# Performance work log

Hardware: AMD Instinct MI355X
Metric: run time of the kernel (lower is better)

Reference implementation:

```python
import jax, jax.numpy as jnp
import numpy as np

B, S, D_IN, D_OUT = 4, 2048, 4096, 4096
N_ADAPTERS, MAX_RANK = 8, 16


def setup_inputs() -> dict:
    key = jax.random.key(0)
    ks = jax.random.split(key, 7)
    x = jax.random.normal(ks[0], (B, S, D_IN), dtype=jnp.float32)
    weight = jax.random.normal(ks[1], (D_OUT, D_IN), dtype=jnp.float32) * (1.0 / np.sqrt(D_IN))
    bias = jax.random.normal(ks[2], (D_OUT,), dtype=jnp.float32) * 0.01
    lora_a_weights = jax.random.normal(ks[3], (N_ADAPTERS, MAX_RANK, D_IN), dtype=jnp.float32) * (1.0 / np.sqrt(D_IN))
    lora_b_weights = jax.random.normal(ks[4], (N_ADAPTERS, D_OUT, MAX_RANK), dtype=jnp.float32) * 0.02
    scaling_factors = jax.random.uniform(ks[5], (N_ADAPTERS,), dtype=jnp.float32, minval=0.5, maxval=2.0)
    adapter_id = jax.random.randint(ks[6], (B,), 0, N_ADAPTERS, dtype=jnp.int64)
    return {
        "x": x,
        "weight": weight,
        "bias": bias,
        "lora_a_weights": lora_a_weights,
        "lora_b_weights": lora_b_weights,
        "scaling_factors": scaling_factors,
        "adapter_id": adapter_id,
    }


def reference(x, weight, bias, lora_a_weights, lora_b_weights, scaling_factors, adapter_id):
    # Base linear: [B,S,Din] @ [Dout,Din]^T + bias -> [B,S,Dout]
    base = jnp.einsum('bsi,oi->bso', x, weight) + bias
    # Per-batch adapter gather (Punica/S-LoRA style bgmv)
    a_sel = lora_a_weights[adapter_id]      # [B, R, Din]
    b_sel = lora_b_weights[adapter_id]      # [B, Dout, R]
    scale = scaling_factors[adapter_id]     # [B]
    low = jnp.einsum('bsi,bri->bsr', x, a_sel)          # [B, S, R]
    delta = jnp.einsum('bsr,bor->bso', low, b_sel)      # [B, S, Dout]
    return base + scale[:, None, None] * delta
```

## Files before the change

### kernel.cpp

```cpp
#include <hip/hip_runtime.h>
#include <hip/hip_bf16.h>

#define BATCH 4
#define SEQ   2048
#define DIN   4096
#define DOUT  4096
#define MTOT  (BATCH * SEQ)
#define RANK  16

typedef __bf16 bf8_t  __attribute__((ext_vector_type(8)));
typedef float  f4_t   __attribute__((ext_vector_type(4)));

#define GLD_LDS(g, l) \
  __builtin_amdgcn_global_load_lds((const __attribute__((address_space(1))) void*)(g), \
                                   (__attribute__((address_space(3))) void*)(l), 16, 0, 0)

__global__ __launch_bounds__(256) void conv_w_kernel(
    const float* __restrict__ w, __bf16* __restrict__ wb) {
  const size_t i = ((size_t)blockIdx.x * 256 + threadIdx.x) * 8;
  f4_t a = *(const f4_t*)(w + i);
  f4_t b = *(const f4_t*)(w + i + 4);
  bf8_t o;
#pragma unroll
  for (int e = 0; e < 4; ++e) { o[e] = (__bf16)a[e]; o[4 + e] = (__bf16)b[e]; }
  *(bf8_t*)(wb + i) = o;
}

__global__ __launch_bounds__(256) void lora_low_kernel(
    const float* __restrict__ x, const float* __restrict__ Aw,
    const float* __restrict__ scales, const int* __restrict__ adapter_id,
    __bf16* __restrict__ xb, float* __restrict__ lowS) {
  const int t    = threadIdx.x;
  const int w    = t >> 6;
  const int lane = t & 63;
  const int quad = lane >> 4;
  const int l16  = lane & 15;
  const int m0   = blockIdx.x * 64;
  const int kb   = blockIdx.y * 512;
  const int b    = adapter_id[m0 >> 11];
  const float scale = scales[b];

  const int row = m0 + w * 16 + l16;
  const float*  xp  = x  + (size_t)row * DIN + kb + quad * 8;
  __bf16*       xbp = xb + (size_t)row * DIN + kb + quad * 8;
  const float*  ap  = Aw + ((size_t)b * RANK + l16) * DIN + kb + quad * 8;

  f4_t acc = (f4_t)0.f;
#pragma unroll 4
  for (int it = 0; it < 16; ++it) {
    const int off = it * 32;
    f4_t u0 = *(const f4_t*)(xp + off);
    f4_t u1 = *(const f4_t*)(xp + off + 4);
    f4_t v0 = *(const f4_t*)(ap + off);
    f4_t v1 = *(const f4_t*)(ap + off + 4);
    bf8_t af, bfr;
#pragma unroll
    for (int e = 0; e < 4; ++e) {
      af[e] = (__bf16)u0[e]; af[4 + e] = (__bf16)u1[e];
      bfr[e] = (__bf16)v0[e]; bfr[4 + e] = (__bf16)v1[e];
    }
    *(bf8_t*)(xbp + off) = af;
    acc = __builtin_amdgcn_mfma_f32_16x16x32_bf16(af, bfr, acc, 0, 0, 0);
  }
#pragma unroll
  for (int e = 0; e < 4; ++e)
    atomicAdd(&lowS[(size_t)(m0 + w * 16 + quad * 4 + e) * RANK + l16], acc[e] * scale);
}

#define BM 256
#define BN 256
#define BKT 64
#define NT (DIN / BKT)
#define NIT (NT / 2)

#define BAR() __builtin_amdgcn_s_barrier()
#define VMW(n) asm volatile("s_waitcnt vmcnt(" #n ")" ::: "memory")

__global__ __launch_bounds__(512, 2) void lora_gemm_kernel(
    const __bf16* __restrict__ x, const __bf16* __restrict__ wgt,
    const float* __restrict__ bias, const float* __restrict__ loraB,
    const int* __restrict__ adapter_id, const float* __restrict__ lowS,
    float* __restrict__ out) {
  __shared__ __bf16 lds[2][2][2][128 * 64];

  const int t    = threadIdx.x;
  const int w    = t >> 6;
  const int lane = t & 63;
  const int quad = lane >> 4;
  const int l16  = lane & 15;
  const int wm   = w >> 2;
  const int wn   = w & 3;

  const int linear = blockIdx.y * 16 + blockIdx.x;
  const int swz = (linear & 7) * 64 + (linear >> 3);
  const int m0 = (swz >> 4) * BM;
  const int n0 = (swz & 15) * BN;

  const int srow = t >> 3;
  const int sc   = (t & 7) ^ ((t >> 4) & 7);
  const __bf16* gA = x   + (size_t)(m0 + srow) * DIN + sc * 8;
  const __bf16* gB = wgt + (size_t)(n0 + srow) * DIN + sc * 8;
  const int ldsw = w * 512;

#define STG(buf, mat, half, kel, gp) do {                                        \
    GLD_LDS((gp) + (size_t)((half) * 128) * DIN + (kel),                         \
            &lds[buf][mat][half][ldsw]);                                         \
    GLD_LDS((gp) + (size_t)((half) * 128 + 64) * DIN + (kel),                    \
            &lds[buf][mat][half][4096 + ldsw]);                                  \
  } while (0)

  const int st0 = (quad ^ ((l16 >> 1) & 7)) * 8;
  const int st1 = ((4 + quad) ^ ((l16 >> 1) & 7)) * 8;

  bf8_t a[4][2], b[2][2];
  f4_t acc[8][4];
#pragma unroll
  for (int i = 0; i < 8; ++i)
#pragma unroll
    for (int j = 0; j < 4; ++j) acc[i][j] = (f4_t)0.f;

#define LDA(buf, mh) do {                                                        \
    const __bf16* base_ = &lds[buf][0][wm][0];                                   \
    _Pragma("unroll")                                                            \
    for (int mq = 0; mq < 4; ++mq) {                                             \
      const int r_ = ((mh) * 4 + mq) * 16 + l16;                                 \
      a[mq][0] = *(const bf8_t*)(base_ + r_ * 64 + st0);                         \
      a[mq][1] = *(const bf8_t*)(base_ + r_ * 64 + st1);                         \
    }                                                                            \
  } while (0)

#define LDB(buf, nh) do {                                                        \
    const __bf16* base_ = &lds[buf][1][wn >> 1][(wn & 1) * 4096];                \
    _Pragma("unroll")                                                            \
    for (int nq = 0; nq < 2; ++nq) {                                             \
      const int r_ = ((nh) * 2 + nq) * 16 + l16;                                 \
      b[nq][0] = *(const bf8_t*)(base_ + r_ * 64 + st0);                         \
      b[nq][1] = *(const bf8_t*)(base_ + r_ * 64 + st1);                         \
    }                                                                            \
  } while (0)

#define MM(mh, nh) do {                                                          \
    __builtin_amdgcn_s_setprio(1);                                               \
    _Pragma("unroll")                                                            \
    for (int ks = 0; ks < 2; ++ks)                                               \
      _Pragma("unroll")                                                          \
      for (int mq = 0; mq < 4; ++mq)                                             \
        _Pragma("unroll")                                                        \
        for (int nq = 0; nq < 2; ++nq)                                           \
          acc[(mh) * 4 + mq][(nh) * 2 + nq] = __builtin_amdgcn_mfma_f32_16x16x32_bf16( \
              a[mq][ks], b[nq][ks], acc[(mh) * 4 + mq][(nh) * 2 + nq], 0, 0, 0); \
    __builtin_amdgcn_s_setprio(0);                                               \
  } while (0)

  STG(0, 0, 0, 0, gA); STG(0, 0, 1, 0, gA);
  STG(0, 1, 0, 0, gB); STG(0, 1, 1, 0, gB);
  STG(1, 0, 0, BKT, gA); STG(1, 1, 1, BKT, gB);
  VMW(4);
  BAR();

  for (int it = 0; it < NIT; ++it) {
    const int k1 = (2 * it + 1) * BKT;
    const int k2 = ((2 * it + 2) & (NT - 1)) * BKT;
    const int k3 = ((2 * it + 3) & (NT - 1)) * BKT;
    LDA(0, 0); LDB(0, 0); STG(1, 1, 0, k1, gB);
    BAR(); MM(0, 0); BAR();
    LDB(0, 1); STG(1, 0, 1, k1, gA);
    BAR(); MM(0, 1); BAR();
    LDA(0, 1); STG(0, 0, 0, k2, gA);
    BAR(); MM(1, 1); BAR();
    LDB(0, 0); STG(0, 1, 1, k2, gB);
    VMW(4);
    BAR(); MM(1, 0); BAR();
    LDA(1, 0); LDB(1, 0); STG(0, 1, 0, k2, gB);
    BAR(); MM(0, 0); BAR();
    LDB(1, 1); STG(0, 0, 1, k2, gA);
    BAR(); MM(0, 1); BAR();
    LDA(1, 1); STG(1, 0, 0, k3, gA);
    BAR(); MM(1, 1); BAR();
    LDB(1, 0); STG(1, 1, 1, k3, gB);
    VMW(4);
    BAR(); MM(1, 0); BAR();
  }
#undef STG
#undef LDA
#undef LDB
#undef MM

  const int b_id = adapter_id[m0 >> 11];
  bf8_t alow[8], blow[4];
  if (quad < 2) {
#pragma unroll
    for (int mf = 0; mf < 8; ++mf) {
      const float* p = &lowS[(size_t)(m0 + wm * 128 + mf * 16 + l16) * RANK + quad * 8];
      f4_t u0 = *(const f4_t*)p;
      f4_t u1 = *(const f4_t*)(p + 4);
#pragma unroll
      for (int e = 0; e < 4; ++e) { alow[mf][e] = (__bf16)u0[e]; alow[mf][4 + e] = (__bf16)u1[e]; }
    }
#pragma unroll
    for (int nf = 0; nf < 4; ++nf) {
      const float* p = &loraB[((size_t)b_id * DOUT + n0 + wn * 64 + nf * 16 + l16) * RANK + quad * 8];
      f4_t u0 = *(const f4_t*)p;
      f4_t u1 = *(const f4_t*)(p + 4);
#pragma unroll
      for (int e = 0; e < 4; ++e) { blow[nf][e] = (__bf16)u0[e]; blow[nf][4 + e] = (__bf16)u1[e]; }
    }
  } else {
#pragma unroll
    for (int i = 0; i < 8; ++i)
#pragma unroll
      for (int e = 0; e < 8; ++e) alow[i][e] = (__bf16)0.f;
#pragma unroll
    for (int j = 0; j < 4; ++j)
#pragma unroll
      for (int e = 0; e < 8; ++e) blow[j][e] = (__bf16)0.f;
  }
#pragma unroll
  for (int mf = 0; mf < 8; ++mf)
#pragma unroll
    for (int nf = 0; nf < 4; ++nf)
      acc[mf][nf] = __builtin_amdgcn_mfma_f32_16x16x32_bf16(alow[mf], blow[nf], acc[mf][nf], 0, 0, 0);

#pragma unroll
  for (int nf = 0; nf < 4; ++nf) {
    const int c = n0 + wn * 64 + nf * 16 + l16;
    const float bc = bias[c];
#pragma unroll
    for (int mf = 0; mf < 8; ++mf) {
      const int r0 = m0 + wm * 128 + mf * 16 + quad * 4;
#pragma unroll
      for (int e = 0; e < 4; ++e)
        out[(size_t)(r0 + e) * DOUT + c] = acc[mf][nf][e] + bc;
    }
  }
}

extern "C" void kernel_launch(void* const* d_in, const int* in_sizes, int n_in,
                              void* d_out, int out_size, void* d_ws, size_t ws_size,
                              hipStream_t stream) {
  const float* x       = (const float*)d_in[0];
  const float* weight  = (const float*)d_in[1];
  const float* bias    = (const float*)d_in[2];
  const float* lora_a  = (const float*)d_in[3];
  const float* lora_b  = (const float*)d_in[4];
  const float* scaling = (const float*)d_in[5];
  const int*   adapter = (const int*)d_in[6];
  float* out = (float*)d_out;

  __bf16* xb   = (__bf16*)d_ws;
  __bf16* wb   = xb + (size_t)MTOT * DIN;
  float*  lowS = (float*)(wb + (size_t)DOUT * DIN);

  hipMemsetAsync(lowS, 0, (size_t)MTOT * RANK * sizeof(float), stream);
  conv_w_kernel<<<(size_t)DOUT * DIN / 8 / 256, 256, 0, stream>>>(weight, wb);
  dim3 lgrid(MTOT / 64, 8);
  lora_low_kernel<<<lgrid, 256, 0, stream>>>(x, lora_a, scaling, adapter, xb, lowS);
  dim3 grid(DOUT / BN, MTOT / BM);
  lora_gemm_kernel<<<grid, 512, 0, stream>>>(xb, wb, bias, lora_b, adapter, lowS, out);
}
```

Measured before the change: 504.0 us.

## Fuse weight conversion and LoRA-low into one prekernel; reorder GEMM staging

Merges the weight bf16 conversion and the x-convert/LoRA-A projection into a single launch: some blocks compute the low-rank product with an in-block LDS reduction instead of atomics, and the remaining blocks convert the weight in a grid-stride loop. This removes the memset and two launches and avoids atomic contention on lowS. The GEMM main loop also regroups its global-to-LDS staging so A halves and B halves are issued at different points of the schedule. Each low-rank block now handles only 16 rows over the full K, so fewer waves work per row block, and the new staging order changes the overlap of loads with the waitcnt points.

```diff
diff --git a/kernel.cpp b/kernel.cpp
--- a/kernel.cpp
+++ b/kernel.cpp
@@ -15,56 +15,65 @@
   __builtin_amdgcn_global_load_lds((const __attribute__((address_space(1))) void*)(g), \
                                    (__attribute__((address_space(3))) void*)(l), 16, 0, 0)
 
-__global__ __launch_bounds__(256) void conv_w_kernel(
-    const float* __restrict__ w, __bf16* __restrict__ wb) {
-  const size_t i = ((size_t)blockIdx.x * 256 + threadIdx.x) * 8;
-  f4_t a = *(const f4_t*)(w + i);
-  f4_t b = *(const f4_t*)(w + i + 4);
-  bf8_t o;
-#pragma unroll
-  for (int e = 0; e < 4; ++e) { o[e] = (__bf16)a[e]; o[4 + e] = (__bf16)b[e]; }
-  *(bf8_t*)(wb + i) = o;
-}
-
-__global__ __launch_bounds__(256) void lora_low_kernel(
-    const float* __restrict__ x, const float* __restrict__ Aw,
-    const float* __restrict__ scales, const int* __restrict__ adapter_id,
-    __bf16* __restrict__ xb, float* __restrict__ lowS) {
-  const int t    = threadIdx.x;
-  const int w    = t >> 6;
-  const int lane = t & 63;
-  const int quad = lane >> 4;
-  const int l16  = lane & 15;
-  const int m0   = blockIdx.x * 64;
-  const int kb   = blockIdx.y * 512;
-  const int b    = adapter_id[m0 >> 11];
-  const float scale = scales[b];
-
-  const int row = m0 + w * 16 + l16;
-  const float*  xp  = x  + (size_t)row * DIN + kb + quad * 8;
-  __bf16*       xbp = xb + (size_t)row * DIN + kb + quad * 8;
-  const float*  ap  = Aw + ((size_t)b * RANK + l16) * DIN + kb + quad * 8;
-
-  f4_t acc = (f4_t)0.f;
+#define LOWBLK 512
+#define PREGRID 2048
+
+__global__ __launch_bounds__(256) void pre_kernel(
+    const float* __restrict__ x, const float* __restrict__ w,
+    const float* __restrict__ Aw, const float* __restrict__ scales,
+    const int* __restrict__ adapter_id,
+    __bf16* __restrict__ xb, __bf16* __restrict__ wb,
+    float* __restrict__ lowS) {
+  const int bid = blockIdx.x;
+  if (bid < LOWBLK) {
+    __shared__ float red[4][16][16];
+    const int t    = threadIdx.x;
+    const int wv   = t >> 6;
+    const int lane = t & 63;
+    const int quad = lane >> 4;
+    const int l16  = lane & 15;
+    const int m0   = bid * 16;
+    const int b    = adapter_id[m0 >> 11];
+    const int kb   = wv * 1024;
+
+    const float*  xp  = x  + (size_t)(m0 + l16) * DIN + kb + quad * 8;
+    __bf16*       xbp = xb + (size_t)(m0 + l16) * DIN + kb + quad * 8;
+    const float*  ap  = Aw + ((size_t)b * RANK + l16) * DIN + kb + quad * 8;
+
+    f4_t acc = (f4_t)0.f;
 #pragma unroll 4
-  for (int it = 0; it < 16; ++it) {
-    const int off = it * 32;
-    f4_t u0 = *(const f4_t*)(xp + off);
-    f4_t u1 = *(const f4_t*)(xp + off + 4);
-    f4_t v0 = *(const f4_t*)(ap + off);
-    f4_t v1 = *(const f4_t*)(ap + off + 4);
-    bf8_t af, bfr;
-#pragma unroll
-    for (int e = 0; e < 4; ++e) {
-      af[e] = (__bf16)u0[e]; af[4 + e] = (__bf16)u1[e];
-      bfr[e] = (__bf16)v0[e]; bfr[4 + e] = (__bf16)v1[e];
-    }
-    *(bf8_t*)(xbp + off) = af;
-    acc = __builtin_amdgcn_mfma_f32_16x16x32_bf16(af, bfr, acc, 0, 0, 0);
-  }
-#pragma unroll
-  for (int e = 0; e < 4; ++e)
-    atomicAdd(&lowS[(size_t)(m0 + w * 16 + quad * 4 + e) * RANK + l16], acc[e] * scale);
+    for (int it = 0; it < 32; ++it) {
+      const int off = it * 32;
+      f4_t u0 = *(const f4_t*)(xp + off);
+      f4_t u1 = *(const f4_t*)(xp + off + 4);
+      f4_t v0 = *(const f4_t*)(ap + off);
+      f4_t v1 = *(const f4_t*)(ap + off + 4);
+      bf8_t af, bfr;
+#pragma unroll
+      for (int e = 0; e < 4; ++e) {
+        af[e] = (__bf16)u0[e]; af[4 + e] = (__bf16)u1[e];
+        bfr[e] = (__bf16)v0[e]; bfr[4 + e] = (__bf16)v1[e];
+      }
+      *(bf8_t*)(xbp + off) = af;
+      acc = __builtin_amdgcn_mfma_f32_16x16x32_bf16(af, bfr, acc, 0, 0, 0);
+    }
+#pragma unroll
+    for (int e = 0; e < 4; ++e) red[wv][quad * 4 + e][l16] = acc[e];
+    __syncthreads();
+    const int r = t >> 4, c = t & 15;
+    const float s = red[0][r][c] + red[1][r][c] + red[2][r][c] + red[3][r][c];
+    lowS[(size_t)(m0 + r) * RANK + c] = s * scales[b];
+  } else {
+    for (int cb = bid - LOWBLK; cb < 8192; cb += PREGRID - LOWBLK) {
+      const size_t i = ((size_t)cb * 256 + threadIdx.x) * 8;
+      f4_t a = *(const f4_t*)(w + i);
+      f4_t bb = *(const f4_t*)(w + i + 4);
+      bf8_t o;
+#pragma unroll
+      for (int e = 0; e < 4; ++e) { o[e] = (__bf16)a[e]; o[4 + e] = (__bf16)bb[e]; }
+      *(bf8_t*)(wb + i) = o;
+    }
+  }
 }
 
 #define BM 256
@@ -102,11 +111,19 @@
   const __bf16* gB = wgt + (size_t)(n0 + srow) * DIN + sc * 8;
   const int ldsw = w * 512;
 
-#define STG(buf, mat, half, kel, gp) do {                                        \
-    GLD_LDS((gp) + (size_t)((half) * 128) * DIN + (kel),                         \
-            &lds[buf][mat][half][ldsw]);                                         \
-    GLD_LDS((gp) + (size_t)((half) * 128 + 64) * DIN + (kel),                    \
-            &lds[buf][mat][half][4096 + ldsw]);                                  \
+#define STG_A_LOW(buf, kel) do {                                                 \
+    GLD_LDS(gA + (kel),                       &lds[buf][0][0][ldsw]);            \
+    GLD_LDS(gA + (size_t)128 * DIN + (kel),   &lds[buf][0][1][ldsw]);            \
+  } while (0)
+#define STG_A_HIGH(buf, kel) do {                                                \
+    GLD_LDS(gA + (size_t)64 * DIN + (kel),    &lds[buf][0][0][4096 + ldsw]);     \
+    GLD_LDS(gA + (size_t)192 * DIN + (kel),   &lds[buf][0][1][4096 + ldsw]);     \
+  } while (0)
+#define STG_B(buf, half, kel) do {                                               \
+    GLD_LDS(gB + (size_t)((half) * 128) * DIN + (kel),                           \
+            &lds[buf][1][half][ldsw]);                                           \
+    GLD_LDS(gB + (size_t)((half) * 128 + 64) * DIN + (kel),                      \
+            &lds[buf][1][half][4096 + ldsw]);                                    \
   } while (0)
 
   const int st0 = (quad ^ ((l16 >> 1) & 7)) * 8;
@@ -152,9 +169,8 @@
     __builtin_amdgcn_s_setprio(0);                                               \
   } while (0)
 
-  STG(0, 0, 0, 0, gA); STG(0, 0, 1, 0, gA);
-  STG(0, 1, 0, 0, gB); STG(0, 1, 1, 0, gB);
-  STG(1, 0, 0, BKT, gA); STG(1, 1, 1, BKT, gB);
+  STG_A_LOW(0, 0); STG_A_HIGH(0, 0); STG_B(0, 0, 0); STG_B(0, 1, 0);
+  STG_A_LOW(1, BKT); STG_A_HIGH(1, BKT);
   VMW(4);
   BAR();
 
@@ -162,26 +178,28 @@
     const int k1 = (2 * it + 1) * BKT;
     const int k2 = ((2 * it + 2) & (NT - 1)) * BKT;
     const int k3 = ((2 * it + 3) & (NT - 1)) * BKT;
-    LDA(0, 0); LDB(0, 0); STG(1, 1, 0, k1, gB);
+    LDA(0, 0); LDB(0, 0); STG_B(1, 0, k1);
     BAR(); MM(0, 0); BAR();
-    LDB(0, 1); STG(1, 0, 1, k1, gA);
+    LDB(0, 1); STG_B(1, 1, k1); STG_A_LOW(0, k2);
     BAR(); MM(0, 1); BAR();
-    LDA(0, 1); STG(0, 0, 0, k2, gA);
+    LDA(0, 1);
     BAR(); MM(1, 1); BAR();
-    LDB(0, 0); STG(0, 1, 1, k2, gB);
+    LDB(0, 0); STG_A_HIGH(0, k2);
     VMW(4);
     BAR(); MM(1, 0); BAR();
-    LDA(1, 0); LDB(1, 0); STG(0, 1, 0, k2, gB);
+    LDA(1, 0); LDB(1, 0); STG_B(0, 0, k2);
     BAR(); MM(0, 0); BAR();
-    LDB(1, 1); STG(0, 0, 1, k2, gA);
+    LDB(1, 1); STG_B(0, 1, k2); STG_A_LOW(1, k3);
     BAR(); MM(0, 1); BAR();
-    LDA(1, 1); STG(1, 0, 0, k3, gA);
+    LDA(1, 1);
     BAR(); MM(1, 1); BAR();
-    LDB(1, 0); STG(1, 1, 1, k3, gB);
+    LDB(1, 0); STG_A_HIGH(1, k3);
     VMW(4);
     BAR(); MM(1, 0); BAR();
   }
-#undef STG
+#undef STG_A_LOW
+#undef STG_A_HIGH
+#undef STG_B
 #undef LDA
 #undef LDB
 #undef MM
@@ -251,10 +269,8 @@
   __bf16* wb   = xb + (size_t)MTOT * DIN;
   float*  lowS = (float*)(wb + (size_t)DOUT * DIN);
 
-  hipMemsetAsync(lowS, 0, (size_t)MTOT * RANK * sizeof(float), stream);
-  conv_w_kernel<<<(size_t)DOUT * DIN / 8 / 256, 256, 0, stream>>>(weight, wb);
-  dim3 lgrid(MTOT / 64, 8);
-  lora_low_kernel<<<lgrid, 256, 0, stream>>>(x, lora_a, scaling, adapter, xb, lowS);
+  pre_kernel<<<PREGRID, 256, 0, stream>>>(x, weight, lora_a, scaling, adapter,
+                                          xb, wb, lowS);
   dim3 grid(DOUT / BN, MTOT / BM);
   lora_gemm_kernel<<<grid, 512, 0, stream>>>(xb, wb, bias, lora_b, adapter, lowS, out);
 }
```

Result: no change. 512.3 us (+1.6%).
